# Performance work log

Hardware: AMD Instinct MI355X
Metric: run time of the kernel (lower is better)

Reference implementation:

```python
import jax, jax.numpy as jnp
import numpy as np

B, CIN, H, W = 1, 128, 448, 512
CLASSES = 128
CR0, CR1 = 128, 4


def setup_inputs() -> dict:
    key = jax.random.key(0)
    ks = jax.random.split(key, 13)
    s = 0.05  # small init scale to keep leaky_relu chain numerically tame
    def rn(k, shape):
        return jax.random.normal(k, shape, dtype=jnp.float32) * s
    return {
        "x_in": jax.random.normal(ks[0], (B, CIN, H, W), dtype=jnp.float32),
        # grouped 1x1 convs, groups=height -> per-height (out, in) matrices
        "w_cl1": rn(ks[1], (H, 128, CIN)), "b_cl1": rn(ks[2], (H, 128)),
        "w_cl2": rn(ks[3], (H, 128, 128)), "b_cl2": rn(ks[4], (H, 128)),
        "w_cl3": rn(ks[5], (H, CLASSES + 1, 128)), "b_cl3": rn(ks[6], (H, CLASSES + 1)),
        "w_reg1": rn(ks[7], (H, CR0, CIN)), "b_reg1": rn(ks[8], (H, CR0)),
        # CondMul expert tables: one small matmul per (height, class) index
        "w2": rn(ks[9], (H * CLASSES, CR0, CR1)), "b2": rn(ks[10], (H * CLASSES, CR1)),
        "w3": rn(ks[11], (H * CLASSES, CR1, 1)), "b3": rn(ks[12], (H * CLASSES, 1)),
    }


def _lrelu(v):
    return jnp.where(v >= 0, v, 0.01 * v)


def _gconv(t, wt, bt):
    # grouped 1x1 conv with groups=height: per-height matmul over channels
    # t: (B,H,Cin,W), wt: (H,Cout,Cin), bt: (H,Cout) -> (B,H,Cout,W)
    return jnp.einsum('bhcw,hoc->bhow', t, wt) + bt[None, :, :, None]


def reference(x_in, w_cl1, b_cl1, w_cl2, b_cl2, w_cl3, b_cl3,
              w_reg1, b_reg1, w2, b2, w3, b3):
    b, _, h, w = x_in.shape
    n_cls = w_cl3.shape[1] - 1
    x = jnp.transpose(x_in, (0, 2, 1, 3))  # (B,H,Cin,W)

    x_r = _lrelu(_gconv(x, w_reg1, b_reg1))  # (B,H,CR0,W)
    t = _lrelu(_gconv(x, w_cl1, b_cl1))
    t = _lrelu(_gconv(t, w_cl2, b_cl2))
    cl = jnp.transpose(_gconv(t, w_cl3, b_cl3), (0, 2, 1, 3))  # (B,classes+1,H,W)

    logits = cl[:, :n_cls]          # (B,classes,H,W)
    mask = _lrelu(cl[:, -1:])       # (B,1,H,W)
    inds = jnp.argmax(logits, axis=1)  # (B,H,W) hard routing

    # indices flattened in (b,h,w) order (as in the original)
    inds_r = (inds + jnp.arange(h)[None, :, None] * n_cls).reshape(-1).astype(jnp.int32)
    rows = jnp.transpose(x_r, (0, 3, 1, 2)).reshape(-1, x_r.shape[2])  # (N,CR0)

    # CondMul: per-row expert gather + tiny matmul + bias
    hdn = _lrelu(jnp.einsum('nc,nco->no', rows, w2[inds_r]) + b2[inds_r])  # (N,CR1)
    r = jnp.einsum('nc,nco->no', hdn, w3[inds_r]) + b3[inds_r]             # (N,1)
    r = jnp.transpose(r.reshape(b, w, h, 1), (0, 3, 2, 1))  # (B,1,H,W)

    x_real = (inds[:, None].astype(jnp.float32) + r) * (1.0 / float(n_cls))
    return (x_real, mask)
```

## Files before the change

kernel.cpp:

```cpp
#include <hip/hip_runtime.h>
#include <hip/hip_bf16.h>

#define HH 448
#define WW 512
#define CHW (HH*WW)
#define NPIX (HH*WW)
#define WCH 128
#define LDW 140
#define WLD 132

typedef unsigned short u16;
typedef __attribute__((ext_vector_type(8))) u16 ushort8v;

__device__ __forceinline__ float lrelu(float v) { return v >= 0.f ? v : 0.01f * v; }

__device__ __forceinline__ u16 f2bf(float v) {
    __hip_bfloat16 b = __float2bfloat16(v);
    union { __hip_bfloat16 h; u16 u; } cv; cv.h = b;
    return cv.u;
}

__device__ __forceinline__ float bf2f(u16 u) {
    union { unsigned int i; float f; } cv; cv.i = ((unsigned int)u) << 16;
    return cv.f;
}

__device__ __forceinline__ int swz8(int g) { return g * 8 + ((g >> 2) << 2); }

template<bool EXTRA>
__device__ __forceinline__ void gemm_phase(
    const float* __restrict__ wsrc, const float* __restrict__ bsrc, int O,
    const float* __restrict__ sbuf, float* __restrict__ wtb, float* __restrict__ biasb,
    float (&acc)[8][8], float& a128, int tid, int o0, int xoff, int swtid)
{
#pragma unroll
    for (int i = 0; i < 8; ++i)
#pragma unroll
        for (int j = 0; j < 8; ++j) acc[i][j] = 0.f;
    a128 = 0.f;

    for (int pan = 0; pan < 8; ++pan) {
        __syncthreads();
#pragma unroll
        for (int it = 0; it < 2; ++it) {
            int slot = it * 256 + tid;
            int kq = slot & 3;
            int o  = slot >> 2;
            const float4 wv = *(const float4*)(wsrc + o * 128 + pan * 16 + kq * 4);
            wtb[(kq * 4 + 0) * WLD + o] = wv.x;
            wtb[(kq * 4 + 1) * WLD + o] = wv.y;
            wtb[(kq * 4 + 2) * WLD + o] = wv.z;
            wtb[(kq * 4 + 3) * WLD + o] = wv.w;
        }
        if (EXTRA && tid < 4) {
            const float4 wv = *(const float4*)(wsrc + 128 * 128 + pan * 16 + tid * 4);
            wtb[(tid * 4 + 0) * WLD + 128] = wv.x;
            wtb[(tid * 4 + 1) * WLD + 128] = wv.y;
            wtb[(tid * 4 + 2) * WLD + 128] = wv.z;
            wtb[(tid * 4 + 3) * WLD + 128] = wv.w;
        }
        if (pan == 0 && tid < O) biasb[tid] = bsrc[tid];
        __syncthreads();

#pragma unroll 4
        for (int kk = 0; kk < 16; ++kk) {
            const int kg = pan * 16 + kk;
            const float4 xa = *(const float4*)(sbuf + kg * LDW + xoff);
            const float4 xb = *(const float4*)(sbuf + kg * LDW + xoff + 4);
            const float4 wa = *(const float4*)(wtb + kk * WLD + o0);
            const float4 wb = *(const float4*)(wtb + kk * WLD + o0 + 4);
            const float xv[8] = {xa.x, xa.y, xa.z, xa.w, xb.x, xb.y, xb.z, xb.w};
            const float wv[8] = {wa.x, wa.y, wa.z, wa.w, wb.x, wb.y, wb.z, wb.w};
#pragma unroll
            for (int i = 0; i < 8; ++i)
#pragma unroll
                for (int j = 0; j < 8; ++j)
                    acc[i][j] = fmaf(wv[i], xv[j], acc[i][j]);
        }
        if (EXTRA && tid < 128) {
#pragma unroll 4
            for (int kk = 0; kk < 16; ++kk)
                a128 = fmaf(wtb[kk * WLD + 128], sbuf[(pan * 16 + kk) * LDW + swtid], a128);
        }
    }
}

__global__ __launch_bounds__(256, 2) void stage1_kernel(
    const float* __restrict__ x_in,
    const float* __restrict__ w_cl1, const float* __restrict__ b_cl1,
    const float* __restrict__ w_cl2, const float* __restrict__ b_cl2,
    const float* __restrict__ w_cl3, const float* __restrict__ b_cl3,
    const float* __restrict__ w_reg1, const float* __restrict__ b_reg1,
    u16* __restrict__ xr_ws, int* __restrict__ inds_ws, float* __restrict__ out)
{
    __shared__ float xs[128 * LDW];
    __shared__ float wtb[16 * WLD];
    __shared__ float biasb[WLD];

    const int tid = threadIdx.x;
    const int b = blockIdx.x;
    const int h     = (b >> 5) * 8 + (b & 7);
    const int chunk = (b >> 3) & 3;
    const int wbase = chunk * WCH;

    const int og = tid >> 4, wg = tid & 15;
    const int o0 = og * 8,  w0 = wg * 8;
    const int xoff  = swz8(wg);
    const int swtid = swz8(tid >> 3) + (tid & 7);

    {
        const float* xg = x_in + h * WW + wbase;
#pragma unroll
        for (int it = 0; it < 16; ++it) {
            int slot = it * 256 + tid;
            int c = slot >> 5, w4 = slot & 31;
            float4 v = *(const float4*)(xg + (size_t)c * CHW + w4 * 4);
            *(float4*)(xs + c * LDW + swz8(w4 >> 1) + (w4 & 1) * 4) = v;
        }
    }

    float acc[8][8]; float a128;

    gemm_phase<false>(w_reg1 + (size_t)h * 16384, b_reg1 + h * 128, 128, xs, wtb, biasb, acc, a128, tid, o0, xoff, swtid);
    {
#pragma unroll
        for (int j = 0; j < 8; ++j) {
            const int n = (wbase + w0 + j) * HH + h;
            ushort8v pk;
#pragma unroll
            for (int i = 0; i < 8; ++i)
                pk[i] = f2bf(lrelu(acc[i][j] + biasb[o0 + i]));
            *(ushort8v*)(xr_ws + (size_t)n * 128 + o0) = pk;
        }
    }

    gemm_phase<false>(w_cl1 + (size_t)h * 16384, b_cl1 + h * 128, 128, xs, wtb, biasb, acc, a128, tid, o0, xoff, swtid);
    __syncthreads();
#pragma unroll
    for (int i = 0; i < 8; ++i) {
        float bo = biasb[o0 + i];
        *(float4*)(xs + (o0 + i) * LDW + xoff) =
            make_float4(lrelu(acc[i][0] + bo), lrelu(acc[i][1] + bo), lrelu(acc[i][2] + bo), lrelu(acc[i][3] + bo));
        *(float4*)(xs + (o0 + i) * LDW + xoff + 4) =
            make_float4(lrelu(acc[i][4] + bo), lrelu(acc[i][5] + bo), lrelu(acc[i][6] + bo), lrelu(acc[i][7] + bo));
    }

    gemm_phase<false>(w_cl2 + (size_t)h * 16384, b_cl2 + h * 128, 128, xs, wtb, biasb, acc, a128, tid, o0, xoff, swtid);
    __syncthreads();
#pragma unroll
    for (int i = 0; i < 8; ++i) {
        float bo = biasb[o0 + i];
        *(float4*)(xs + (o0 + i) * LDW + xoff) =
            make_float4(lrelu(acc[i][0] + bo), lrelu(acc[i][1] + bo), lrelu(acc[i][2] + bo), lrelu(acc[i][3] + bo));
        *(float4*)(xs + (o0 + i) * LDW + xoff + 4) =
            make_float4(lrelu(acc[i][4] + bo), lrelu(acc[i][5] + bo), lrelu(acc[i][6] + bo), lrelu(acc[i][7] + bo));
    }

    gemm_phase<true>(w_cl3 + (size_t)h * 16512, b_cl3 + h * 129, 129, xs, wtb, biasb, acc, a128, tid, o0, xoff, swtid);

    __syncthreads();
    float* sval = xs;
    int*   sidx = (int*)(xs + 2048);
#pragma unroll
    for (int j = 0; j < 8; ++j) {
        float bv = -3.4e38f; int bi = 0;
#pragma unroll
        for (int i = 0; i < 8; ++i) {
            float v = acc[i][j] + biasb[o0 + i];
            if (v > bv) { bv = v; bi = o0 + i; }
        }
        sval[og * 128 + (w0 + j)] = bv;
        sidx[og * 128 + (w0 + j)] = bi;
    }
    __syncthreads();
    if (tid < 128) {
        const int w = tid;
        float bv = sval[w]; int bi = sidx[w];
#pragma unroll
        for (int g = 1; g < 16; ++g) {
            float v = sval[g * 128 + w];
            if (v > bv) { bv = v; bi = sidx[g * 128 + w]; }
        }
        inds_ws[h * WW + wbase + w] = bi;
        out[NPIX + h * WW + wbase + w] = lrelu(a128 + biasb[128]);
    }
}

__global__ __launch_bounds__(256, 4) void stage2_kernel(
    const u16* __restrict__ xr_ws, const int* __restrict__ inds_ws,
    const float* __restrict__ w2g, const float* __restrict__ b2g,
    const float* __restrict__ w3g, const float* __restrict__ b3g,
    float* __restrict__ out)
{
    const int lane = threadIdx.x & 63;
    const int n = blockIdx.x * 4 + (threadIdx.x >> 6);
    const unsigned un = (unsigned)n;
    const int h = un % 448u, w = un / 448u;
    const int idx = inds_ws[n] + ((n >> 9) << 7);

    const int c0 = lane << 1;
    const u16* rp = xr_ws + (size_t)n * 128 + c0;
    const float r0 = bf2f(rp[0]), r1 = bf2f(rp[1]);

    const float* wrow = w2g + (size_t)idx * 512;
    const float4 wa = *(const float4*)(wrow + (c0 << 2));
    const float4 wb = *(const float4*)(wrow + (c0 << 2) + 4);

    float s0 = r0 * wa.x + r1 * wb.x;
    float s1 = r0 * wa.y + r1 * wb.y;
    float s2 = r0 * wa.z + r1 * wb.z;
    float s3 = r0 * wa.w + r1 * wb.w;
#pragma unroll
    for (int m = 1; m < 64; m <<= 1) {
        s0 += __shfl_xor(s0, m, 64);
        s1 += __shfl_xor(s1, m, 64);
        s2 += __shfl_xor(s2, m, 64);
        s3 += __shfl_xor(s3, m, 64);
    }
    if (lane == 0) {
        const float4 b2v = *(const float4*)(b2g + (idx << 2));
        const float4 w3v = *(const float4*)(w3g + (idx << 2));
        float rr = b3g[idx];
        rr += lrelu(s0 + b2v.x) * w3v.x;
        rr += lrelu(s1 + b2v.y) * w3v.y;
        rr += lrelu(s2 + b2v.z) * w3v.z;
        rr += lrelu(s3 + b2v.w) * w3v.w;
        const int p = h * WW + w;
        const float ind_local = (float)inds_ws[p];
        out[p] = (ind_local + rr) * 0.0078125f;
    }
}

extern "C" void kernel_launch(void* const* d_in, const int* in_sizes, int n_in,
                              void* d_out, int out_size, void* d_ws, size_t ws_size,
                              hipStream_t stream)
{
    const float* x_in   = (const float*)d_in[0];
    const float* w_cl1  = (const float*)d_in[1];
    const float* b_cl1  = (const float*)d_in[2];
    const float* w_cl2  = (const float*)d_in[3];
    const float* b_cl2  = (const float*)d_in[4];
    const float* w_cl3  = (const float*)d_in[5];
    const float* b_cl3  = (const float*)d_in[6];
    const float* w_reg1 = (const float*)d_in[7];
    const float* b_reg1 = (const float*)d_in[8];
    const float* w2     = (const float*)d_in[9];
    const float* b2     = (const float*)d_in[10];
    const float* w3     = (const float*)d_in[11];
    const float* b3     = (const float*)d_in[12];

    float* out = (float*)d_out;
    u16* xr_ws = (u16*)d_ws;
    int* inds  = (int*)((char*)d_ws + (size_t)NPIX * 128 * 2);

    stage1_kernel<<<dim3(448 * 4), dim3(256), 0, stream>>>(
        x_in, w_cl1, b_cl1, w_cl2, b_cl2, w_cl3, b_cl3, w_reg1, b_reg1,
        xr_ws, inds, out);

    stage2_kernel<<<dim3(NPIX / 4), dim3(256), 0, stream>>>(
        xr_ws, inds, w2, b2, w3, b3, out);
}
```

Before: 709.4 us.

## Load per-height weights directly from global memory instead of staging panels in LDS

The 1x1 grouped-conv GEMM phases no longer stage 16-wide weight panels through a transposed shared-memory tile with two barriers per panel. Each thread now reads its own 8 output rows of weights straight from global memory as float4 (cached in L1/L2) and applies them to 4 k-steps of activations from LDS. This removes 16 barriers per phase and the LDS transpose writes. In exchange, weight traffic becomes uncoalesced per-thread global loads, duplicated across the 16 threads that share an output group, which adds memory latency and raises register pressure.

Result: faster. 671.5 us (-5.3%).

```diff
diff --git a/kernel.cpp b/kernel.cpp
--- a/kernel.cpp
+++ b/kernel.cpp
@@ -7,7 +7,6 @@
 #define NPIX (HH*WW)
 #define WCH 128
 #define LDW 140
-#define WLD 132
 
 typedef unsigned short u16;
 typedef __attribute__((ext_vector_type(8))) u16 ushort8v;
@@ -30,7 +29,7 @@
 template<bool EXTRA>
 __device__ __forceinline__ void gemm_phase(
     const float* __restrict__ wsrc, const float* __restrict__ bsrc, int O,
-    const float* __restrict__ sbuf, float* __restrict__ wtb, float* __restrict__ biasb,
+    const float* __restrict__ xs, float* __restrict__ biasb,
     float (&acc)[8][8], float& a128, int tid, int o0, int xoff, int swtid)
 {
 #pragma unroll
@@ -39,50 +38,47 @@
         for (int j = 0; j < 8; ++j) acc[i][j] = 0.f;
     a128 = 0.f;
 
-    for (int pan = 0; pan < 8; ++pan) {
-        __syncthreads();
-#pragma unroll
-        for (int it = 0; it < 2; ++it) {
-            int slot = it * 256 + tid;
-            int kq = slot & 3;
-            int o  = slot >> 2;
-            const float4 wv = *(const float4*)(wsrc + o * 128 + pan * 16 + kq * 4);
-            wtb[(kq * 4 + 0) * WLD + o] = wv.x;
-            wtb[(kq * 4 + 1) * WLD + o] = wv.y;
-            wtb[(kq * 4 + 2) * WLD + o] = wv.z;
-            wtb[(kq * 4 + 3) * WLD + o] = wv.w;
-        }
-        if (EXTRA && tid < 4) {
-            const float4 wv = *(const float4*)(wsrc + 128 * 128 + pan * 16 + tid * 4);
-            wtb[(tid * 4 + 0) * WLD + 128] = wv.x;
-            wtb[(tid * 4 + 1) * WLD + 128] = wv.y;
-            wtb[(tid * 4 + 2) * WLD + 128] = wv.z;
-            wtb[(tid * 4 + 3) * WLD + 128] = wv.w;
-        }
-        if (pan == 0 && tid < O) biasb[tid] = bsrc[tid];
-        __syncthreads();
-
-#pragma unroll 4
-        for (int kk = 0; kk < 16; ++kk) {
-            const int kg = pan * 16 + kk;
-            const float4 xa = *(const float4*)(sbuf + kg * LDW + xoff);
-            const float4 xb = *(const float4*)(sbuf + kg * LDW + xoff + 4);
-            const float4 wa = *(const float4*)(wtb + kk * WLD + o0);
-            const float4 wb = *(const float4*)(wtb + kk * WLD + o0 + 4);
-            const float xv[8] = {xa.x, xa.y, xa.z, xa.w, xb.x, xb.y, xb.z, xb.w};
-            const float wv[8] = {wa.x, wa.y, wa.z, wa.w, wb.x, wb.y, wb.z, wb.w};
-#pragma unroll
-            for (int i = 0; i < 8; ++i)
+    __syncthreads();
+    if (tid < O) biasb[tid] = bsrc[tid];
+
+    const float* wb   = wsrc + o0 * 128;
+    const float* w128 = wsrc + 128 * 128;
+
+#pragma unroll 2
+    for (int k4 = 0; k4 < 32; ++k4) {
+        float4 wv[8];
+#pragma unroll
+        for (int i = 0; i < 8; ++i)
+            wv[i] = *(const float4*)(wb + i * 128 + k4 * 4);
+        float4 xva[4], xvb[4];
+#pragma unroll
+        for (int r = 0; r < 4; ++r) {
+            xva[r] = *(const float4*)(xs + (k4 * 4 + r) * LDW + xoff);
+            xvb[r] = *(const float4*)(xs + (k4 * 4 + r) * LDW + xoff + 4);
+        }
+#pragma unroll
+        for (int r = 0; r < 4; ++r) {
+            const float xr8[8] = {xva[r].x, xva[r].y, xva[r].z, xva[r].w,
+                                  xvb[r].x, xvb[r].y, xvb[r].z, xvb[r].w};
+#pragma unroll
+            for (int i = 0; i < 8; ++i) {
+                const float ws4[4] = {wv[i].x, wv[i].y, wv[i].z, wv[i].w};
+                const float wi = ws4[r];
 #pragma unroll
                 for (int j = 0; j < 8; ++j)
-                    acc[i][j] = fmaf(wv[i], xv[j], acc[i][j]);
+                    acc[i][j] = fmaf(wi, xr8[j], acc[i][j]);
+            }
         }
         if (EXTRA && tid < 128) {
-#pragma unroll 4
-            for (int kk = 0; kk < 16; ++kk)
-                a128 = fmaf(wtb[kk * WLD + 128], sbuf[(pan * 16 + kk) * LDW + swtid], a128);
-        }
-    }
+            const float4 w4 = *(const float4*)(w128 + k4 * 4);
+            a128 = fmaf(w4.x, xs[(k4 * 4 + 0) * LDW + swtid], a128);
+            a128 = fmaf(w4.y, xs[(k4 * 4 + 1) * LDW + swtid], a128);
+            a128 = fmaf(w4.z, xs[(k4 * 4 + 2) * LDW + swtid], a128);
+            a128 = fmaf(w4.w, xs[(k4 * 4 + 3) * LDW + swtid], a128);
+        }
+    }
+
+    __syncthreads();
 }
 
 __global__ __launch_bounds__(256, 2) void stage1_kernel(
@@ -94,8 +90,7 @@
     u16* __restrict__ xr_ws, int* __restrict__ inds_ws, float* __restrict__ out)
 {
     __shared__ float xs[128 * LDW];
-    __shared__ float wtb[16 * WLD];
-    __shared__ float biasb[WLD];
+    __shared__ float biasb[132];
 
     const int tid = threadIdx.x;
     const int b = blockIdx.x;
@@ -121,7 +116,7 @@
 
     float acc[8][8]; float a128;
 
-    gemm_phase<false>(w_reg1 + (size_t)h * 16384, b_reg1 + h * 128, 128, xs, wtb, biasb, acc, a128, tid, o0, xoff, swtid);
+    gemm_phase<false>(w_reg1 + (size_t)h * 16384, b_reg1 + h * 128, 128, xs, biasb, acc, a128, tid, o0, xoff, swtid);
     {
 #pragma unroll
         for (int j = 0; j < 8; ++j) {
@@ -134,8 +129,7 @@
         }
     }
 
-    gemm_phase<false>(w_cl1 + (size_t)h * 16384, b_cl1 + h * 128, 128, xs, wtb, biasb, acc, a128, tid, o0, xoff, swtid);
-    __syncthreads();
+    gemm_phase<false>(w_cl1 + (size_t)h * 16384, b_cl1 + h * 128, 128, xs, biasb, acc, a128, tid, o0, xoff, swtid);
 #pragma unroll
     for (int i = 0; i < 8; ++i) {
         float bo = biasb[o0 + i];
@@ -145,8 +139,7 @@
             make_float4(lrelu(acc[i][4] + bo), lrelu(acc[i][5] + bo), lrelu(acc[i][6] + bo), lrelu(acc[i][7] + bo));
     }
 
-    gemm_phase<false>(w_cl2 + (size_t)h * 16384, b_cl2 + h * 128, 128, xs, wtb, biasb, acc, a128, tid, o0, xoff, swtid);
-    __syncthreads();
+    gemm_phase<false>(w_cl2 + (size_t)h * 16384, b_cl2 + h * 128, 128, xs, biasb, acc, a128, tid, o0, xoff, swtid);
 #pragma unroll
     for (int i = 0; i < 8; ++i) {
         float bo = biasb[o0 + i];
@@ -156,9 +149,8 @@
             make_float4(lrelu(acc[i][4] + bo), lrelu(acc[i][5] + bo), lrelu(acc[i][6] + bo), lrelu(acc[i][7] + bo));
     }
 
-    gemm_phase<true>(w_cl3 + (size_t)h * 16512, b_cl3 + h * 129, 129, xs, wtb, biasb, acc, a128, tid, o0, xoff, swtid);
-
-    __syncthreads();
+    gemm_phase<true>(w_cl3 + (size_t)h * 16512, b_cl3 + h * 129, 129, xs, biasb, acc, a128, tid, o0, xoff, swtid);
+
     float* sval = xs;
     int*   sidx = (int*)(xs + 2048);
 #pragma unroll
```
